# Performance work log

Measured on AMD Instinct MI355X. Metric: run time of the kernel, lower is better.

The kernel has to match this reference:

```python
import jax, jax.numpy as jnp
import numpy as np

KERNEL = (3, 3, 3, 3)
PAD = (1, 1, 1, 1)
IN_CH = 8
OUT_CH = 8


def setup_inputs() -> dict:
    key = jax.random.key(0)
    k1, k2, k3 = jax.random.split(key, 3)
    x = jax.random.normal(k1, (2, IN_CH, 7, 7, 48, 48), dtype=jnp.float32)
    K = KERNEL[0] * KERNEL[1] * KERNEL[2] * KERNEL[3]
    conv = jax.random.normal(k2, (OUT_CH, K * IN_CH), dtype=jnp.float32) * 0.05
    bias = jax.random.normal(k3, (OUT_CH,), dtype=jnp.float32) * 0.05
    return {"x": x, "conv": conv, "bias": bias}


def reference(x, conv, bias):
    # x: (B, C, u, v, h, w); conv: (oc, k0*k1*k2*k3*C); bias: (oc,)
    B, C, u, v, h, w = x.shape
    oc = conv.shape[0]
    k0, k1, k2, k3 = KERNEL
    # torch unfold+permute orders the contraction axis as (k0,k1,k2,k3,C)
    W = conv.reshape(oc, k0, k1, k2, k3, C)
    xp = jnp.pad(x, ((0, 0), (0, 0),
                     (PAD[0], PAD[0]), (PAD[1], PAD[1]),
                     (PAD[2], PAD[2]), (PAD[3], PAD[3])))
    out = jnp.zeros((B, oc, u, v, h, w), dtype=x.dtype)
    # stride = 1 everywhere: accumulate over the 3^4 kernel offsets
    for i0 in range(k0):
        for i1 in range(k1):
            for i2 in range(k2):
                for i3 in range(k3):
                    xs = xp[:, :, i0:i0 + u, i1:i1 + v, i2:i2 + h, i3:i3 + w]
                    out = out + jnp.einsum('bcuvhw,oc->bouvhw', xs,
                                           W[:, i0, i1, i2, i3, :])
    out = out + bias[None, :, None, None, None, None]
    return out
```

## Files before the change

### kernel.cpp

```cpp
#include <hip/hip_runtime.h>


typedef __attribute__((ext_vector_type(8))) short short8;
typedef __attribute__((ext_vector_type(4))) float f32x4;

#define CSTRIDE (49 * 2304)
#define XP_BYTES 3920000
#define ZS_OFF   3920000
#define WP_OFF   3960000

__device__ __forceinline__ unsigned short f2bf(float f) {
    union { float f; unsigned u; } v; v.f = f;
    unsigned u = v.u;
    return (unsigned short)((u + 0x7FFF + ((u >> 16) & 1)) >> 16);
}

__global__ __launch_bounds__(256)
void prep_x(const float* __restrict__ x, unsigned short* __restrict__ ws16) {
    int g = blockIdx.x * 256 + threadIdx.x;
    if (g >= 247500) return;
    unsigned short vals[8];
#pragma unroll
    for (int c = 0; c < 8; ++c) vals[c] = 0;
    if (g < 245000) {
        int b  = g / 122500;
        int r  = g - b * 122500;
        int uv = r / 2500;
        int p  = r - uv * 2500;
        int hh = p / 50, ww = p - hh * 50;
        int h = hh - 1, w = ww - 1;
        if (((unsigned)h < 48u) && ((unsigned)w < 48u)) {
            const float* xb = x + ((size_t)b * 8 * 49 + uv) * 2304 + h * 48 + w;
#pragma unroll
            for (int c = 0; c < 8; ++c) vals[c] = f2bf(xb[(size_t)c * CSTRIDE]);
        }
    }
    *(short8*)(ws16 + (size_t)g * 8) = *(const short8*)vals;
}

__global__ __launch_bounds__(256)
void prep_w(const float* __restrict__ conv, unsigned short* __restrict__ wp) {
    int i = blockIdx.x * 256 + threadIdx.x;
    if (i >= 10752) return;
    int chunk = i >> 9;
    int rem   = i & 511;
    int lane  = rem >> 3, j = rem & 7;
    int m = lane & 15, q = lane >> 4;
    int tap = chunk * 4 + q;
    unsigned short v = 0;
    if (m < 8 && tap < 81) v = f2bf(conv[m * 648 + tap * 8 + j]);
    wp[i] = v;
}

__global__ __launch_bounds__(256, 4)
void conv4d_mfma(const unsigned short* __restrict__ ws16,
                 const float* __restrict__ bias,
                 float* __restrict__ out) {
    __shared__ int taboff[84];

    const int img = blockIdx.y;
    const int b   = img / 49;
    const int uvr = img - b * 49;
    const int u   = uvr / 7;
    const int v   = uvr - u * 7;

    if (threadIdx.x < 84) {
        int tap = threadIdx.x;
        int i0 = tap / 27, r = tap - i0 * 27;
        int i1 = r / 9;    r -= i1 * 9;
        int i2 = r / 3,    i3 = r - i2 * 3;
        int uu = u + i0 - 1, vv = v + i1 - 1;
        bool valid = (tap < 81) && ((unsigned)uu < 7u) && ((unsigned)vv < 7u);
        int so = valid ? (((b * 7 + uu) * 7 + vv) * 2500) * 16 : ZS_OFF;
        taboff[tap] = so + (i2 * 50 + i3) * 16;
    }
    __syncthreads();

    const int lane = threadIdx.x & 63;
    const int wave = threadIdx.x >> 6;
    const int n    = lane & 15;
    const int quad = lane >> 4;
    const int sbase = blockIdx.x * 256 + wave * 64;

    int myoff[4];
#pragma unroll
    for (int t = 0; t < 4; ++t) {
        int s = sbase + t * 16 + n;
        int h = s / 48, w = s - h * 48;
        myoff[t] = (h * 50 + w) * 16;
    }

    const char* xpb = (const char*)ws16;
    const char* wpb = xpb + WP_OFF;

    f32x4 acc[4];
#pragma unroll
    for (int t = 0; t < 4; ++t) acc[t] = (f32x4){0.f, 0.f, 0.f, 0.f};

    for (int chunk = 0; chunk < 21; ++chunk) {
        short8 wf = *(const short8*)(wpb + chunk * 1024 + lane * 16);
        int toff  = taboff[chunk * 4 + quad];
        const char* base = xpb + toff;
#pragma unroll
        for (int t = 0; t < 4; ++t) {
            short8 xf = *(const short8*)(base + myoff[t]);
            acc[t] = __builtin_amdgcn_mfma_f32_16x16x32_bf16(wf, xf, acc[t], 0, 0, 0);
        }
    }

    if (quad < 2) {
        f32x4 bb = *(const f32x4*)(bias + quad * 4);
        float* ob = out + ((size_t)b * 8 * 49 + uvr) * 2304;
#pragma unroll
        for (int t = 0; t < 4; ++t) {
            int s = sbase + t * 16 + n;
#pragma unroll
            for (int r = 0; r < 4; ++r) {
                int o = quad * 4 + r;
                ob[(size_t)o * CSTRIDE + s] = acc[t][r] + bb[r];
            }
        }
    }
}

extern "C" void kernel_launch(void* const* d_in, const int* in_sizes, int n_in,
                              void* d_out, int out_size, void* d_ws, size_t ws_size,
                              hipStream_t stream) {
    const float* x    = (const float*)d_in[0];
    const float* conv = (const float*)d_in[1];
    const float* bias = (const float*)d_in[2];
    float* out = (float*)d_out;
    unsigned short* ws16 = (unsigned short*)d_ws;

    prep_x<<<dim3((247500 + 255) / 256), dim3(256), 0, stream>>>(x, ws16);
    prep_w<<<dim3((10752 + 255) / 256), dim3(256), 0, stream>>>(conv, ws16 + WP_OFF / 2);
    conv4d_mfma<<<dim3(9, 98), dim3(256), 0, stream>>>(ws16, bias, out);
}
```

Measured before the change: 80.65 us.

## Skip out-of-bounds uv taps, stage weights in LDS, merge prep kernels

The conv kernel now builds a per-block list of only the valid (u,v) neighbour taps and runs a variable number of MFMA chunks, instead of always running 21 chunks over a zero buffer. Weights are repacked per tap and copied into LDS, then indexed through a per-slot weight offset table. The two prep kernels are merged into one launch to cut launch overhead. In exchange each block pays for an LDS weight copy, an extra sync, and serial tap enumeration on thread 0.

```diff
diff --git a/kernel.cpp b/kernel.cpp
--- a/kernel.cpp
+++ b/kernel.cpp
@@ -3,11 +3,12 @@
 
 typedef __attribute__((ext_vector_type(8))) short short8;
 typedef __attribute__((ext_vector_type(4))) float f32x4;
+typedef __attribute__((ext_vector_type(4))) int   i32x4;
 
 #define CSTRIDE (49 * 2304)
-#define XP_BYTES 3920000
 #define ZS_OFF   3920000
 #define WP_OFF   3960000
+#define WP_BYTES 20992
 
 __device__ __forceinline__ unsigned short f2bf(float f) {
     union { float f; unsigned u; } v; v.f = f;
@@ -16,47 +17,49 @@
 }
 
 __global__ __launch_bounds__(256)
-void prep_x(const float* __restrict__ x, unsigned short* __restrict__ ws16) {
+void prep(const float* __restrict__ x, const float* __restrict__ conv,
+          unsigned short* __restrict__ ws16) {
     int g = blockIdx.x * 256 + threadIdx.x;
-    if (g >= 247500) return;
-    unsigned short vals[8];
+    if (g < 247500) {
+        unsigned short vals[8];
 #pragma unroll
-    for (int c = 0; c < 8; ++c) vals[c] = 0;
-    if (g < 245000) {
-        int b  = g / 122500;
-        int r  = g - b * 122500;
-        int uv = r / 2500;
-        int p  = r - uv * 2500;
-        int hh = p / 50, ww = p - hh * 50;
-        int h = hh - 1, w = ww - 1;
-        if (((unsigned)h < 48u) && ((unsigned)w < 48u)) {
-            const float* xb = x + ((size_t)b * 8 * 49 + uv) * 2304 + h * 48 + w;
+        for (int c = 0; c < 8; ++c) vals[c] = 0;
+        if (g < 245000) {
+            int b  = g / 122500;
+            int r  = g - b * 122500;
+            int uv = r / 2500;
+            int p  = r - uv * 2500;
+            int hh = p / 50, ww = p - hh * 50;
+            int h = hh - 1, w = ww - 1;
+            if (((unsigned)h < 48u) && ((unsigned)w < 48u)) {
+                const float* xb = x + ((size_t)b * 8 * 49 + uv) * 2304 + h * 48 + w;
 #pragma unroll
-            for (int c = 0; c < 8; ++c) vals[c] = f2bf(xb[(size_t)c * CSTRIDE]);
+                for (int c = 0; c < 8; ++c) vals[c] = f2bf(xb[(size_t)c * CSTRIDE]);
+            }
+        }
+        *(short8*)(ws16 + (size_t)g * 8) = *(const short8*)vals;
+    } else {
+        int i = g - 247500;
+        if (i < 10496) {
+            int tap = i >> 7;
+            int r   = i & 127;
+            int m   = r >> 3, j = r & 7;
+            unsigned short v = 0;
+            if (tap < 81 && m < 8) v = f2bf(conv[m * 648 + tap * 8 + j]);
+            ws16[WP_OFF / 2 + i] = v;
         }
     }
-    *(short8*)(ws16 + (size_t)g * 8) = *(const short8*)vals;
-}
-
-__global__ __launch_bounds__(256)
-void prep_w(const float* __restrict__ conv, unsigned short* __restrict__ wp) {
-    int i = blockIdx.x * 256 + threadIdx.x;
-    if (i >= 10752) return;
-    int chunk = i >> 9;
-    int rem   = i & 511;
-    int lane  = rem >> 3, j = rem & 7;
-    int m = lane & 15, q = lane >> 4;
-    int tap = chunk * 4 + q;
-    unsigned short v = 0;
-    if (m < 8 && tap < 81) v = f2bf(conv[m * 648 + tap * 8 + j]);
-    wp[i] = v;
 }
 
 __global__ __launch_bounds__(256, 4)
 void conv4d_mfma(const unsigned short* __restrict__ ws16,
                  const float* __restrict__ bias,
                  float* __restrict__ out) {
-    __shared__ int taboff[84];
+    __shared__ unsigned short wlds[WP_BYTES / 2];
+    __shared__ int taboff_s[84];
+    __shared__ int woff_s[84];
+    __shared__ int s_vt[9];
+    __shared__ int s_nv;
 
     const int img = blockIdx.y;
     const int b   = img / 49;
@@ -64,22 +67,47 @@
     const int u   = uvr / 7;
     const int v   = uvr - u * 7;
 
-    if (threadIdx.x < 84) {
-        int tap = threadIdx.x;
-        int i0 = tap / 27, r = tap - i0 * 27;
-        int i1 = r / 9;    r -= i1 * 9;
-        int i2 = r / 3,    i3 = r - i2 * 3;
-        int uu = u + i0 - 1, vv = v + i1 - 1;
-        bool valid = (tap < 81) && ((unsigned)uu < 7u) && ((unsigned)vv < 7u);
-        int so = valid ? (((b * 7 + uu) * 7 + vv) * 2500) * 16 : ZS_OFF;
-        taboff[tap] = so + (i2 * 50 + i3) * 16;
+    {
+        const i32x4* wsrc = (const i32x4*)((const char*)ws16 + WP_OFF);
+        i32x4* wdst = (i32x4*)wlds;
+        for (int i = threadIdx.x; i < WP_BYTES / 16; i += 256) wdst[i] = wsrc[i];
+    }
+
+    if (threadIdx.x == 0) {
+        int nv = 0;
+        for (int i01 = 0; i01 < 9; ++i01) {
+            int i0 = i01 / 3, i1 = i01 - 3 * i0;
+            int uu = u + i0 - 1, vv = v + i1 - 1;
+            if (((unsigned)uu < 7u) && ((unsigned)vv < 7u)) s_vt[nv++] = i01;
+        }
+        s_nv = nv;
     }
     __syncthreads();
 
-    const int lane = threadIdx.x & 63;
-    const int wave = threadIdx.x >> 6;
-    const int n    = lane & 15;
-    const int quad = lane >> 4;
+    const int nv     = s_nv;
+    const int nchunk = (nv * 9 + 3) >> 2;
+
+    if (threadIdx.x < 84) {
+        int s = threadIdx.x;
+        if (s < nv * 9) {
+            int g9  = s / 9, hw9 = s - 9 * g9;
+            int i01 = s_vt[g9];
+            int i0 = i01 / 3, i1 = i01 - 3 * i0;
+            int i2 = hw9 / 3, i3 = hw9 - 3 * i2;
+            int uu = u + i0 - 1, vv = v + i1 - 1;
+            taboff_s[s] = ((((b * 7 + uu) * 7 + vv) * 2500) + i2 * 50 + i3) * 16;
+            woff_s[s]   = (i01 * 9 + hw9) * 256;
+        } else if (s < 84) {
+            taboff_s[s] = ZS_OFF;
+            woff_s[s]   = 81 * 256;
+        }
+    }
+    __syncthreads();
+
+    const int lane  = threadIdx.x & 63;
+    const int wave  = threadIdx.x >> 6;
+    const int n     = lane & 15;
+    const int quad  = lane >> 4;
     const int sbase = blockIdx.x * 256 + wave * 64;
 
     int myoff[4];
@@ -91,15 +119,17 @@
     }
 
     const char* xpb = (const char*)ws16;
-    const char* wpb = xpb + WP_OFF;
+    const char* wld = (const char*)wlds;
 
     f32x4 acc[4];
 #pragma unroll
     for (int t = 0; t < 4; ++t) acc[t] = (f32x4){0.f, 0.f, 0.f, 0.f};
 
-    for (int chunk = 0; chunk < 21; ++chunk) {
-        short8 wf = *(const short8*)(wpb + chunk * 1024 + lane * 16);
-        int toff  = taboff[chunk * 4 + quad];
+    for (int c = 0; c < nchunk; ++c) {
+        int slot = 4 * c + quad;
+        int toff = taboff_s[slot];
+        int woff = woff_s[slot];
+        short8 wf = *(const short8*)(wld + woff + n * 16);
         const char* base = xpb + toff;
 #pragma unroll
         for (int t = 0; t < 4; ++t) {
@@ -132,7 +162,6 @@
     float* out = (float*)d_out;
     unsigned short* ws16 = (unsigned short*)d_ws;
 
-    prep_x<<<dim3((247500 + 255) / 256), dim3(256), 0, stream>>>(x, ws16);
-    prep_w<<<dim3((10752 + 255) / 256), dim3(256), 0, stream>>>(conv, ws16 + WP_OFF / 2);
+    prep<<<dim3((247500 + 10496 + 255) / 256), dim3(256), 0, stream>>>(x, conv, ws16);
     conv4d_mfma<<<dim3(9, 98), dim3(256), 0, stream>>>(ws16, bias, out);
 }
```

Measured after the change: 79.44 us. Within noise of the previous version (-1.5%).

## Skip out-of-range u/v taps via precomputed per-image tap table, fuse prep kernels

Applied to the files above, without the earlier changes.

Prep kernels are merged into one launch that also builds, for each (b,u,v) image, a compact table of valid tap offsets and weight offsets. The conv kernel then loops only over the valid taps for that image and no longer multiplies zero-padded u/v boundary taps. It also drops the shared-memory tap table and its barrier, shrinks blocks to 128 threads with 2 tiles per wave, and software-prefetches the next chunk's operands. The cost is more blocks, a per-chunk global table load, and a tail of up to three padding taps that point to a zeroed weight slot.

```diff
diff --git a/kernel.cpp b/kernel.cpp
--- a/kernel.cpp
+++ b/kernel.cpp
@@ -3,11 +3,11 @@
 
 typedef __attribute__((ext_vector_type(8))) short short8;
 typedef __attribute__((ext_vector_type(4))) float f32x4;
+typedef __attribute__((ext_vector_type(2))) int   i32x2;
 
 #define CSTRIDE (49 * 2304)
-#define XP_BYTES 3920000
-#define ZS_OFF   3920000
-#define WP_OFF   3960000
+#define WP_OFF  3920000
+#define WT_OFF  3940992
 
 __device__ __forceinline__ unsigned short f2bf(float f) {
     union { float f; unsigned u; } v; v.f = f;
@@ -16,13 +16,13 @@
 }
 
 __global__ __launch_bounds__(256)
-void prep_x(const float* __restrict__ x, unsigned short* __restrict__ ws16) {
+void prep(const float* __restrict__ x, const float* __restrict__ conv,
+          unsigned short* __restrict__ ws16) {
     int g = blockIdx.x * 256 + threadIdx.x;
-    if (g >= 247500) return;
-    unsigned short vals[8];
+    if (g < 245000) {
+        unsigned short vals[8];
 #pragma unroll
-    for (int c = 0; c < 8; ++c) vals[c] = 0;
-    if (g < 245000) {
+        for (int c = 0; c < 8; ++c) vals[c] = 0;
         int b  = g / 122500;
         int r  = g - b * 122500;
         int uv = r / 2500;
@@ -34,91 +34,104 @@
 #pragma unroll
             for (int c = 0; c < 8; ++c) vals[c] = f2bf(xb[(size_t)c * CSTRIDE]);
         }
+        *(short8*)(ws16 + (size_t)g * 8) = *(const short8*)vals;
+        return;
     }
-    *(short8*)(ws16 + (size_t)g * 8) = *(const short8*)vals;
+    g -= 245000;
+    if (g < 10496) {
+        int tap = g >> 7;
+        int r   = g & 127;
+        int m   = r >> 3, j = r & 7;
+        unsigned short v = 0;
+        if (tap < 81 && m < 8) v = f2bf(conv[m * 648 + tap * 8 + j]);
+        ws16[WP_OFF / 2 + g] = v;
+        return;
+    }
+    g -= 10496;
+    if (g < 8624) {
+        int img  = g / 88, slot = g - img * 88;
+        int b    = img / 49, uv = img - b * 49;
+        int u    = uv / 7,   v  = uv - u * 7;
+        int cu = 3 - (u == 0) - (u == 6);
+        int cv = 3 - (v == 0) - (v == 6);
+        int tab, wof;
+        if (slot < cu * cv * 9) {
+            int g9  = slot / 9, hw9 = slot - 9 * g9;
+            int gi0 = g9 / cv,  gi1 = g9 - cv * gi0;
+            int i0 = (u == 0) + gi0, i1 = (v == 0) + gi1;
+            int uu = u + i0 - 1,     vv = v + i1 - 1;
+            int i2 = hw9 / 3,        i3 = hw9 - 3 * i2;
+            tab = (((b * 7 + uu) * 7 + vv) * 2500 + i2 * 50 + i3) * 16;
+            wof = ((i0 * 3 + i1) * 9 + hw9) * 256;
+        } else {
+            tab = 0;
+            wof = 81 * 256;
+        }
+        i32x2 e; e.x = tab; e.y = wof;
+        *(i32x2*)((char*)ws16 + WT_OFF + (size_t)g * 8) = e;
+    }
 }
 
-__global__ __launch_bounds__(256)
-void prep_w(const float* __restrict__ conv, unsigned short* __restrict__ wp) {
-    int i = blockIdx.x * 256 + threadIdx.x;
-    if (i >= 10752) return;
-    int chunk = i >> 9;
-    int rem   = i & 511;
-    int lane  = rem >> 3, j = rem & 7;
-    int m = lane & 15, q = lane >> 4;
-    int tap = chunk * 4 + q;
-    unsigned short v = 0;
-    if (m < 8 && tap < 81) v = f2bf(conv[m * 648 + tap * 8 + j]);
-    wp[i] = v;
-}
-
-__global__ __launch_bounds__(256, 4)
+__global__ __launch_bounds__(128, 6)
 void conv4d_mfma(const unsigned short* __restrict__ ws16,
                  const float* __restrict__ bias,
                  float* __restrict__ out) {
-    __shared__ int taboff[84];
-
     const int img = blockIdx.y;
     const int b   = img / 49;
     const int uvr = img - b * 49;
     const int u   = uvr / 7;
     const int v   = uvr - u * 7;
+    const int cu  = 3 - (u == 0) - (u == 6);
+    const int cv  = 3 - (v == 0) - (v == 6);
+    const int nchunk = (cu * cv * 9 + 3) >> 2;
 
-    if (threadIdx.x < 84) {
-        int tap = threadIdx.x;
-        int i0 = tap / 27, r = tap - i0 * 27;
-        int i1 = r / 9;    r -= i1 * 9;
-        int i2 = r / 3,    i3 = r - i2 * 3;
-        int uu = u + i0 - 1, vv = v + i1 - 1;
-        bool valid = (tap < 81) && ((unsigned)uu < 7u) && ((unsigned)vv < 7u);
-        int so = valid ? (((b * 7 + uu) * 7 + vv) * 2500) * 16 : ZS_OFF;
-        taboff[tap] = so + (i2 * 50 + i3) * 16;
-    }
-    __syncthreads();
+    const int lane  = threadIdx.x & 63;
+    const int wave  = threadIdx.x >> 6;
+    const int n     = lane & 15;
+    const int quad  = lane >> 4;
+    const int sbase = blockIdx.x * 64 + wave * 32;
 
-    const int lane = threadIdx.x & 63;
-    const int wave = threadIdx.x >> 6;
-    const int n    = lane & 15;
-    const int quad = lane >> 4;
-    const int sbase = blockIdx.x * 256 + wave * 64;
-
-    int myoff[4];
-#pragma unroll
-    for (int t = 0; t < 4; ++t) {
-        int s = sbase + t * 16 + n;
-        int h = s / 48, w = s - h * 48;
-        myoff[t] = (h * 50 + w) * 16;
+    int myoff0, myoff1;
+    {
+        int s0 = sbase + n;
+        int h0 = s0 / 48, w0 = s0 - h0 * 48;
+        myoff0 = (h0 * 50 + w0) * 16;
+        int s1 = sbase + 16 + n;
+        int h1 = s1 / 48, w1 = s1 - h1 * 48;
+        myoff1 = (h1 * 50 + w1) * 16;
     }
 
-    const char* xpb = (const char*)ws16;
-    const char* wpb = xpb + WP_OFF;
+    const char* base0 = (const char*)ws16;
+    const char* wpb   = base0 + WP_OFF;
+    const i32x2* tbl  = (const i32x2*)(base0 + WT_OFF) + img * 88;
+    const int n16     = n * 16;
 
-    f32x4 acc[4];
-#pragma unroll
-    for (int t = 0; t < 4; ++t) acc[t] = (f32x4){0.f, 0.f, 0.f, 0.f};
+    i32x2 tw = tbl[quad];
+    short8 wf  = *(const short8*)(wpb + tw.y + n16);
+    short8 xf0 = *(const short8*)(base0 + tw.x + myoff0);
+    short8 xf1 = *(const short8*)(base0 + tw.x + myoff1);
 
-    for (int chunk = 0; chunk < 21; ++chunk) {
-        short8 wf = *(const short8*)(wpb + chunk * 1024 + lane * 16);
-        int toff  = taboff[chunk * 4 + quad];
-        const char* base = xpb + toff;
-#pragma unroll
-        for (int t = 0; t < 4; ++t) {
-            short8 xf = *(const short8*)(base + myoff[t]);
-            acc[t] = __builtin_amdgcn_mfma_f32_16x16x32_bf16(wf, xf, acc[t], 0, 0, 0);
-        }
+    f32x4 acc0 = (f32x4){0.f, 0.f, 0.f, 0.f};
+    f32x4 acc1 = acc0;
+
+    for (int c = 0; c < nchunk; ++c) {
+        i32x2 twn = tbl[4 * (c + 1) + quad];
+        short8 wfn  = *(const short8*)(wpb + twn.y + n16);
+        short8 xf0n = *(const short8*)(base0 + twn.x + myoff0);
+        short8 xf1n = *(const short8*)(base0 + twn.x + myoff1);
+        acc0 = __builtin_amdgcn_mfma_f32_16x16x32_bf16(wf, xf0, acc0, 0, 0, 0);
+        acc1 = __builtin_amdgcn_mfma_f32_16x16x32_bf16(wf, xf1, acc1, 0, 0, 0);
+        wf = wfn; xf0 = xf0n; xf1 = xf1n;
     }
 
     if (quad < 2) {
         f32x4 bb = *(const f32x4*)(bias + quad * 4);
-        float* ob = out + ((size_t)b * 8 * 49 + uvr) * 2304;
+        float* ob = out + ((size_t)b * 8 * 49 + uvr) * 2304 + sbase + n;
 #pragma unroll
-        for (int t = 0; t < 4; ++t) {
-            int s = sbase + t * 16 + n;
-#pragma unroll
-            for (int r = 0; r < 4; ++r) {
-                int o = quad * 4 + r;
-                ob[(size_t)o * CSTRIDE + s] = acc[t][r] + bb[r];
-            }
+        for (int r = 0; r < 4; ++r) {
+            int o = quad * 4 + r;
+            ob[(size_t)o * CSTRIDE]      = acc0[r] + bb[r];
+            ob[(size_t)o * CSTRIDE + 16] = acc1[r] + bb[r];
         }
     }
 }
@@ -132,7 +145,6 @@
     float* out = (float*)d_out;
     unsigned short* ws16 = (unsigned short*)d_ws;
 
-    prep_x<<<dim3((247500 + 255) / 256), dim3(256), 0, stream>>>(x, ws16);
-    prep_w<<<dim3((10752 + 255) / 256), dim3(256), 0, stream>>>(conv, ws16 + WP_OFF / 2);
-    conv4d_mfma<<<dim3(9, 98), dim3(256), 0, stream>>>(ws16, bias, out);
+    prep<<<dim3((245000 + 10496 + 8624 + 255) / 256), dim3(256), 0, stream>>>(x, conv, ws16);
+    conv4d_mfma<<<dim3(36, 98), dim3(128), 0, stream>>>(ws16, bias, out);
 }
```

After: 82.31 us. 2.1% more time.

## Skip out-of-bounds uv taps, repack MFMA tiles as row pairs, merge prep kernels

Applied to the files above, without the earlier changes.

Merges the x and weight preparation kernels into a single launch, which also builds a per-image table of valid (u,v) neighbour slices. The convolution kernel now iterates only over valid outer taps, with 3 taps per chunk where the MFMA M dimension pairs two output rows. This avoids MFMA work and loads on padded zero slices at the u/v borders. It also removes the shared-memory table and its barrier, and halves block size for more blocks. Each wave now does less work, so there are more waves, and the branching chunk count varies across images.

```diff
diff --git a/kernel.cpp b/kernel.cpp
--- a/kernel.cpp
+++ b/kernel.cpp
@@ -5,9 +5,9 @@
 typedef __attribute__((ext_vector_type(4))) float f32x4;
 
 #define CSTRIDE (49 * 2304)
-#define XP_BYTES 3920000
-#define ZS_OFF   3920000
-#define WP_OFF   3960000
+#define ZS_OFF  3920000
+#define WP_OFF  3960000
+#define WT_OFF  3987648
 
 __device__ __forceinline__ unsigned short f2bf(float f) {
     union { float f; unsigned u; } v; v.f = f;
@@ -16,109 +16,140 @@
 }
 
 __global__ __launch_bounds__(256)
-void prep_x(const float* __restrict__ x, unsigned short* __restrict__ ws16) {
+void prep(const float* __restrict__ x, const float* __restrict__ conv,
+          unsigned short* __restrict__ ws16) {
     int g = blockIdx.x * 256 + threadIdx.x;
-    if (g >= 247500) return;
-    unsigned short vals[8];
+    if (g < 247500) {
+        unsigned short vals[8];
 #pragma unroll
-    for (int c = 0; c < 8; ++c) vals[c] = 0;
-    if (g < 245000) {
-        int b  = g / 122500;
-        int r  = g - b * 122500;
-        int uv = r / 2500;
-        int p  = r - uv * 2500;
-        int hh = p / 50, ww = p - hh * 50;
-        int h = hh - 1, w = ww - 1;
-        if (((unsigned)h < 48u) && ((unsigned)w < 48u)) {
-            const float* xb = x + ((size_t)b * 8 * 49 + uv) * 2304 + h * 48 + w;
+        for (int c = 0; c < 8; ++c) vals[c] = 0;
+        if (g < 245000) {
+            int b  = g / 122500;
+            int r  = g - b * 122500;
+            int uv = r / 2500;
+            int p  = r - uv * 2500;
+            int hh = p / 50, ww = p - hh * 50;
+            int h = hh - 1, w = ww - 1;
+            if (((unsigned)h < 48u) && ((unsigned)w < 48u)) {
+                const float* xb = x + ((size_t)b * 8 * 49 + uv) * 2304 + h * 48 + w;
 #pragma unroll
-            for (int c = 0; c < 8; ++c) vals[c] = f2bf(xb[(size_t)c * CSTRIDE]);
+                for (int c = 0; c < 8; ++c) vals[c] = f2bf(xb[(size_t)c * CSTRIDE]);
+            }
         }
+        *(short8*)(ws16 + (size_t)g * 8) = *(const short8*)vals;
+        return;
     }
-    *(short8*)(ws16 + (size_t)g * 8) = *(const short8*)vals;
+    g -= 247500;
+    if (g < 13824) {
+        int as   = g >> 9;
+        int r    = g & 511;
+        int lane = r >> 3, j = r & 7;
+        int m = lane & 15, q = lane >> 4;
+        int o = m & 7, d = m >> 3;
+        int i0i1 = as / 3, i3 = as - 3 * i0i1;
+        int i2 = q - d;
+        unsigned short v = 0;
+        if ((unsigned)i2 < 3u)
+            v = f2bf(conv[o * 648 + ((i0i1 * 3 + i2) * 3 + i3) * 8 + j]);
+        ws16[WP_OFF / 2 + g] = v;
+        return;
+    }
+    g -= 13824;
+    if (g < 882) {
+        int img = g / 9, k = g - img * 9;
+        int b   = img / 49, uv = img - b * 49;
+        int u   = uv / 7,   v  = uv - u * 7;
+        int entry = ZS_OFF;
+        int cnt = 0;
+        for (int i01 = 0; i01 < 9; ++i01) {
+            int i0 = i01 / 3, i1 = i01 - 3 * i0;
+            int uu = u + i0 - 1, vv = v + i1 - 1;
+            if (((unsigned)uu < 7u) && ((unsigned)vv < 7u)) {
+                if (cnt == k)
+                    entry = (((b * 7 + uu) * 7 + vv) * 40000) | (i01 << 22);
+                ++cnt;
+            }
+        }
+        ((int*)((char*)ws16 + WT_OFF))[g] = entry;
+    }
 }
 
-__global__ __launch_bounds__(256)
-void prep_w(const float* __restrict__ conv, unsigned short* __restrict__ wp) {
-    int i = blockIdx.x * 256 + threadIdx.x;
-    if (i >= 10752) return;
-    int chunk = i >> 9;
-    int rem   = i & 511;
-    int lane  = rem >> 3, j = rem & 7;
-    int m = lane & 15, q = lane >> 4;
-    int tap = chunk * 4 + q;
-    unsigned short v = 0;
-    if (m < 8 && tap < 81) v = f2bf(conv[m * 648 + tap * 8 + j]);
-    wp[i] = v;
-}
-
-__global__ __launch_bounds__(256, 4)
+__global__ __launch_bounds__(128, 4)
 void conv4d_mfma(const unsigned short* __restrict__ ws16,
                  const float* __restrict__ bias,
                  float* __restrict__ out) {
-    __shared__ int taboff[84];
-
     const int img = blockIdx.y;
     const int b   = img / 49;
     const int uvr = img - b * 49;
     const int u   = uvr / 7;
     const int v   = uvr - u * 7;
-
-    if (threadIdx.x < 84) {
-        int tap = threadIdx.x;
-        int i0 = tap / 27, r = tap - i0 * 27;
-        int i1 = r / 9;    r -= i1 * 9;
-        int i2 = r / 3,    i3 = r - i2 * 3;
-        int uu = u + i0 - 1, vv = v + i1 - 1;
-        bool valid = (tap < 81) && ((unsigned)uu < 7u) && ((unsigned)vv < 7u);
-        int so = valid ? (((b * 7 + uu) * 7 + vv) * 2500) * 16 : ZS_OFF;
-        taboff[tap] = so + (i2 * 50 + i3) * 16;
-    }
-    __syncthreads();
+    const int cu  = 3 - (u == 0) - (u == 6);
+    const int cv  = 3 - (v == 0) - (v == 6);
+    const int nchunk = cu * cv * 3;
 
     const int lane = threadIdx.x & 63;
     const int wave = threadIdx.x >> 6;
     const int n    = lane & 15;
     const int quad = lane >> 4;
-    const int sbase = blockIdx.x * 256 + wave * 64;
 
-    int myoff[4];
+    const int widx = blockIdx.x * 2 + wave;
+    const int dt0  = widx * 2;
+    const int rp0  = dt0 / 3,        w00 = (dt0 - 3 * rp0) * 16;
+    const int dt1  = dt0 + 1;
+    const int rp1  = dt1 / 3,        w01 = (dt1 - 3 * rp1) * 16;
+
+    const int myoff0 = ((rp0 * 2 + quad) * 50 + w00 + n) * 16;
+    const int myoff1 = ((rp1 * 2 + quad) * 50 + w01 + n) * 16;
+
+    const char* base0  = (const char*)ws16;
+    const char* wpb    = base0 + WP_OFF;
+    const int   lane16 = lane * 16;
+
+    const int* tblp = (const int*)(base0 + WT_OFF) + img * 9;
+    int t[9];
 #pragma unroll
-    for (int t = 0; t < 4; ++t) {
-        int s = sbase + t * 16 + n;
-        int h = s / 48, w = s - h * 48;
-        myoff[t] = (h * 50 + w) * 16;
+    for (int k = 0; k < 9; ++k) t[k] = tblp[k];
+
+    f32x4 acc0 = (f32x4){0.f, 0.f, 0.f, 0.f};
+    f32x4 acc1 = acc0;
+
+#define CHUNK(c)                                                               \
+    {                                                                          \
+        int sl = (c) / 3, i3 = (c) % 3;                                        \
+        int e   = t[sl];                                                       \
+        int tab = (e & 0x3FFFFF) + i3 * 16;                                    \
+        int wof = (((e >> 22) * 3 + i3) << 10);                                \
+        short8 wf  = *(const short8*)(wpb + wof + lane16);                     \
+        const char* xb = base0 + tab;                                          \
+        short8 xf0 = *(const short8*)(xb + myoff0);                            \
+        short8 xf1 = *(const short8*)(xb + myoff1);                            \
+        acc0 = __builtin_amdgcn_mfma_f32_16x16x32_bf16(wf, xf0, acc0, 0, 0, 0);\
+        acc1 = __builtin_amdgcn_mfma_f32_16x16x32_bf16(wf, xf1, acc1, 0, 0, 0);\
     }
 
-    const char* xpb = (const char*)ws16;
-    const char* wpb = xpb + WP_OFF;
-
-    f32x4 acc[4];
 #pragma unroll
-    for (int t = 0; t < 4; ++t) acc[t] = (f32x4){0.f, 0.f, 0.f, 0.f};
-
-    for (int chunk = 0; chunk < 21; ++chunk) {
-        short8 wf = *(const short8*)(wpb + chunk * 1024 + lane * 16);
-        int toff  = taboff[chunk * 4 + quad];
-        const char* base = xpb + toff;
+    for (int c = 0; c < 12; ++c) CHUNK(c);
+    if (nchunk > 12) {
 #pragma unroll
-        for (int t = 0; t < 4; ++t) {
-            short8 xf = *(const short8*)(base + myoff[t]);
-            acc[t] = __builtin_amdgcn_mfma_f32_16x16x32_bf16(wf, xf, acc[t], 0, 0, 0);
+        for (int c = 12; c < 18; ++c) CHUNK(c);
+        if (nchunk > 18) {
+#pragma unroll
+            for (int c = 18; c < 27; ++c) CHUNK(c);
         }
     }
+#undef CHUNK
 
-    if (quad < 2) {
-        f32x4 bb = *(const f32x4*)(bias + quad * 4);
-        float* ob = out + ((size_t)b * 8 * 49 + uvr) * 2304;
+    {
+        const int d  = quad >> 1;
+        const int oq = (quad & 1) * 4;
+        const f32x4 bb = *(const f32x4*)(bias + oq);
+        float* obase = out + ((size_t)(b * 8 + oq) * 49 + uvr) * 2304;
+        float* ob0 = obase + (rp0 * 2 + d) * 48 + w00 + n;
+        float* ob1 = obase + (rp1 * 2 + d) * 48 + w01 + n;
 #pragma unroll
-        for (int t = 0; t < 4; ++t) {
-            int s = sbase + t * 16 + n;
-#pragma unroll
-            for (int r = 0; r < 4; ++r) {
-                int o = quad * 4 + r;
-                ob[(size_t)o * CSTRIDE + s] = acc[t][r] + bb[r];
-            }
+        for (int r = 0; r < 4; ++r) {
+            ob0[(size_t)r * CSTRIDE] = acc0[r] + bb[r];
+            ob1[(size_t)r * CSTRIDE] = acc1[r] + bb[r];
         }
     }
 }
@@ -132,7 +163,6 @@
     float* out = (float*)d_out;
     unsigned short* ws16 = (unsigned short*)d_ws;
 
-    prep_x<<<dim3((247500 + 255) / 256), dim3(256), 0, stream>>>(x, ws16);
-    prep_w<<<dim3((10752 + 255) / 256), dim3(256), 0, stream>>>(conv, ws16 + WP_OFF / 2);
-    conv4d_mfma<<<dim3(9, 98), dim3(256), 0, stream>>>(ws16, bias, out);
+    prep<<<dim3((247500 + 13824 + 882 + 255) / 256), dim3(256), 0, stream>>>(x, conv, ws16);
+    conv4d_mfma<<<dim3(18, 98), dim3(128), 0, stream>>>(ws16, bias, out);
 }
```

Result: faster. 74.75 us (median of 2 runs) (-7.3%).
